# Performance work log

Measured on AMD Instinct MI355X. Metric: run time of the kernel, lower is better.

## Reference

```python
import jax, jax.numpy as jnp
import numpy as np

INPUT_SIZE = 416.0
CONF_THRESH = 0.25
IOU_THRESH = 0.45
N = 8192


def setup_inputs() -> dict:
    key = jax.random.key(0)
    preds = jax.random.normal(key, (1, 5, N), dtype=jnp.float32)
    return {"preds": preds}


def _pairwise_iou(b):
    # b: [N,4] xyxy -> iou: [N,N], matching the torch clamp(min=0) semantics
    xx1 = jnp.maximum(b[:, None, 0], b[None, :, 0])
    yy1 = jnp.maximum(b[:, None, 1], b[None, :, 1])
    xx2 = jnp.minimum(b[:, None, 2], b[None, :, 2])
    yy2 = jnp.minimum(b[:, None, 3], b[None, :, 3])
    inter = jnp.clip(xx2 - xx1, 0.0) * jnp.clip(yy2 - yy1, 0.0)
    area = jnp.clip(b[:, 2] - b[:, 0], 0.0) * jnp.clip(b[:, 3] - b[:, 1], 0.0)  # [N]
    union = area[:, None] + area[None, :] - inter
    return jnp.where(union > 0, inter / union, 0.0)


def reference(preds):
    # decode: preds [1,5,N] rows = (cx, cy, w, h, obj)
    p = preds[0].T  # [N,5]
    cx, cy, pw, ph, obj = p[:, 0], p[:, 1], p[:, 2], p[:, 3], p[:, 4]
    x1 = cx - pw * 0.5
    y1 = cy - ph * 0.5
    x2 = cx + pw * 0.5
    y2 = cy + ph * 0.5
    boxes = jnp.stack([x1, y1, x2, y2], axis=1)  # [N,4]
    scores = obj
    classes = jnp.zeros_like(scores)

    valid = scores > CONF_THRESH  # conf filter (kept as mask; invalid boxes never kept)
    # scale to absolute coords iff all coords are normalized (max <= 1)
    scale = jnp.where(jnp.max(boxes) <= 1.0, INPUT_SIZE, 1.0)
    boxes_abs = boxes * scale

    # greedy NMS over score-descending order
    order = jnp.argsort(-scores)
    b = boxes_abs[order]          # [N,4]
    s = scores[order]             # [N]
    v = valid[order]              # [N]
    c = classes[order]            # [N]

    iou = _pairwise_iou(b)        # [N,N]

    def step(suppressed, xs):
        iou_row, v_i, i = xs
        keep_i = v_i & jnp.logical_not(suppressed[i])
        suppressed = suppressed | (keep_i & (iou_row > IOU_THRESH))
        return suppressed, keep_i

    _, keep = jax.lax.scan(
        step,
        jnp.zeros((N,), dtype=bool),
        (iou, v, jnp.arange(N)),
    )  # keep: [N] bool, in sorted order

    out = jnp.stack(
        [b[:, 0] / INPUT_SIZE, b[:, 1] / INPUT_SIZE,
         b[:, 2] / INPUT_SIZE, b[:, 3] / INPUT_SIZE, s, c],
        axis=1,
    )  # [N,6]
    # fixed-shape jit-compatible output: suppressed/filtered rows are zeroed;
    # kept rows appear in descending-score order (same order torch compacts to)
    return jnp.where(keep[:, None], out, 0.0)
```

## Files before the change

### kernel.cpp

```cpp
#include <hip/hip_runtime.h>
#include <stdint.h>

typedef unsigned long long u64;
typedef unsigned int u32;

#define NBOX 8192
#define ACMAX 1024
#define NCH 16
#define CONF 0.25f
#define IOU_T 0.45f

#define OFF_CX1    256
#define OFF_CY1    (OFF_CX1 + ACMAX * 4)
#define OFF_CX2    (OFF_CX1 + 2 * ACMAX * 4)
#define OFF_CY2    (OFF_CX1 + 3 * ACMAX * 4)
#define OFF_CSC    (OFF_CX1 + 4 * ACMAX * 4)
#define OFF_CAR    (OFF_CX1 + 5 * ACMAX * 4)
#define OFF_ROFC   (OFF_CX1 + 6 * ACMAX * 4)
#define OFF_CMASKT (OFF_CX1 + 7 * ACMAX * 4)

__device__ inline u32 encf(float f) {
    u32 u = __float_as_uint(f);
    return (u & 0x80000000u) ? ~u : (u | 0x80000000u);
}

__global__ void __launch_bounds__(1024) k_sort(
        const float* __restrict__ p,
        float* __restrict__ cx1, float* __restrict__ cy1,
        float* __restrict__ cx2, float* __restrict__ cy2,
        float* __restrict__ csc, float* __restrict__ car,
        int* __restrict__ rofc, float* __restrict__ out) {
    #pragma clang fp contract(off)
    int t = threadIdx.x;
    int b = blockIdx.x;
    __shared__ u64 keys[9216];
    __shared__ u32 accs[128][36];
    __shared__ u32 accs2[8][32];
    __shared__ float redm[16];
    __shared__ float s_gmax;

    int il4 = (t & 7) * 4;
    int js  = t >> 3;
    int ibase = b * 32;

    u64 Ki[4];
    #pragma unroll
    for (int q = 0; q < 4; q++) {
        int i = ibase + il4 + q;
        u32 e = encf(p[4 * NBOX + i]);
        Ki[q] = ((u64)e << 32) | ((u64)(8191 - i) << 19) | 0x1FFFFull;
    }

    float mloc = -3.4e38f;
    #pragma unroll
    for (int w = 0; w < 8; w++) {
        int j = w * 1024 + t;
        float cxj = p[j], cyj = p[NBOX + j];
        float pwj = p[2 * NBOX + j], phj = p[3 * NBOX + j];
        float sj = p[4 * NBOX + j];
        float hx = pwj * 0.5f, hy = phj * 0.5f;
        float x1 = cxj - hx, y1 = cyj - hy, x2 = cxj + hx, y2 = cyj + hy;
        bool act = (sj > CONF) && (x2 > x1) && (y2 > y1);
        mloc = fmaxf(mloc, fmaxf(fmaxf(x1, y1), fmaxf(x2, y2)));
        u32 e = encf(sj);
        u32 mult = act ? 65537u : 1u;
        keys[j + (j >> 3)] =
            ((u64)e << 32) | ((u64)(8191 - j) << 19) | (u64)mult;
    }
    __syncthreads();

    u32 acc[4] = {0u, 0u, 0u, 0u};
    int base = js * 9;
    #pragma unroll
    for (int w = 0; w < 8; w++) {
        #pragma unroll
        for (int m = 0; m < 8; m++) {
            u64 kj = keys[base + w * 1152 + m];
            u32 mm = (u32)kj & 0x1FFFFu;
            acc[0] += (kj > Ki[0]) ? mm : 0u;
            acc[1] += (kj > Ki[1]) ? mm : 0u;
            acc[2] += (kj > Ki[2]) ? mm : 0u;
            acc[3] += (kj > Ki[3]) ? mm : 0u;
        }
    }
    #pragma unroll
    for (int q = 0; q < 4; q++) accs[js][il4 + q] = acc[q];
    #pragma unroll
    for (int o = 32; o > 0; o >>= 1) mloc = fmaxf(mloc, __shfl_xor(mloc, o, 64));
    if ((t & 63) == 0) redm[t >> 6] = mloc;
    __syncthreads();
    if (t < 256) {
        int il = t & 31, part = t >> 5;
        u32 s = 0;
        #pragma unroll
        for (int q = 0; q < 16; q++) s += accs[part * 16 + q][il];
        accs2[part][il] = s;
    }
    if (t == 0) {
        float g = redm[0];
        #pragma unroll
        for (int k = 1; k < 16; k++) g = fmaxf(g, redm[k]);
        s_gmax = g;
    }
    __syncthreads();
    if (t < 32) {
        u32 total = 0;
        #pragma unroll
        for (int part = 0; part < 8; part++) total += accs2[part][t];
        int r = (int)(total & 0xFFFFu);
        int cr = (int)(total >> 16);
        int i = ibase + t;
        float scale = (s_gmax <= 1.0f) ? 416.0f : 1.0f;
        float cx = p[i], cy = p[NBOX + i];
        float pw = p[2 * NBOX + i], ph = p[3 * NBOX + i];
        float s = p[4 * NBOX + i];
        float hx = pw * 0.5f, hy = ph * 0.5f;
        float x1 = cx - hx, y1 = cy - hy, x2 = cx + hx, y2 = cy + hy;
        bool a = (s > CONF) && (x2 > x1) && (y2 > y1);
        float bx1 = x1 * scale, by1 = y1 * scale;
        float bx2 = x2 * scale, by2 = y2 * scale;
        float aw = fmaxf(bx2 - bx1, 0.0f);
        float ah = fmaxf(by2 - by1, 0.0f);
        float area = aw * ah;
        bool ok = a && (cr < ACMAX);
        if (ok) {
            cx1[cr] = bx1; cy1[cr] = by1; cx2[cr] = bx2; cy2[cr] = by2;
            csc[cr] = s; car[cr] = area; rofc[cr] = r;
        } else {
            bool valid = s > CONF;
            float* o = out + (size_t)r * 6;
            o[0] = valid ? bx1 / 416.0f : 0.0f;
            o[1] = valid ? by1 / 416.0f : 0.0f;
            o[2] = valid ? bx2 / 416.0f : 0.0f;
            o[3] = valid ? by2 / 416.0f : 0.0f;
            o[4] = valid ? s : 0.0f;
            o[5] = 0.0f;
        }
    }
}

__global__ void __launch_bounds__(64) k_mask(
        const float* __restrict__ cx1, const float* __restrict__ cy1,
        const float* __restrict__ cx2, const float* __restrict__ cy2,
        const float* __restrict__ car, const float* __restrict__ csc,
        u64* __restrict__ cmaskT) {
    #pragma clang fp contract(off)
    int t = threadIdx.x;
    int i0 = blockIdx.x * 64, j0 = blockIdx.y * 64;
    u64 rv = __ballot(csc[i0 + t] > CONF);
    u64 cv = __ballot(csc[j0 + t] > CONF);
    if (rv == 0ull || cv == 0ull) return;
    __shared__ float sx1[64], sy1[64], sx2[64], sy2[64], sa[64];
    sx1[t] = cx1[i0 + t]; sy1[t] = cy1[i0 + t];
    sx2[t] = cx2[i0 + t]; sy2[t] = cy2[i0 + t];
    sa[t] = car[i0 + t];
    __syncthreads();
    int j = j0 + t;
    float xj1 = cx1[j], yj1 = cy1[j], xj2 = cx2[j], yj2 = cy2[j], aj = car[j];
    u64 w = 0;
    for (int ii = 0; ii < 64; ii++) {
        float xx1 = fmaxf(sx1[ii], xj1);
        float yy1 = fmaxf(sy1[ii], yj1);
        float xx2 = fminf(sx2[ii], xj2);
        float yy2 = fminf(sy2[ii], yj2);
        float iw = fmaxf(xx2 - xx1, 0.0f);
        float ih = fmaxf(yy2 - yy1, 0.0f);
        float inter = iw * ih;
        float uni = sa[ii] + aj - inter;
        bool sup = (uni > 0.0f) && (inter / uni > IOU_T);
        w |= ((u64)(sup ? 1u : 0u)) << ii;
    }
    cmaskT[(size_t)blockIdx.x * ACMAX + j] = w;
}

__global__ void __launch_bounds__(1024) k_final(
        const float* __restrict__ csc, const u64* __restrict__ cmaskT,
        const float* __restrict__ cx1, const float* __restrict__ cy1,
        const float* __restrict__ cx2, const float* __restrict__ cy2,
        const int* __restrict__ rofc, float* __restrict__ out) {
    int t = threadIdx.x;
    __shared__ u64 keptArr[NCH];
    int wv = t >> 6;
    int j = t & 63;
    float s = csc[t];
    bool valid = s > CONF;
    u64 col[NCH];
    #pragma unroll
    for (int w = 0; w < NCH; w++) col[w] = cmaskT[(size_t)w * ACMAX + t];
    u64 validm = __ballot(valid);
    if (j == 0) keptArr[wv] = validm;
    __syncthreads();
    u64 below = (j == 0) ? 0ull : (~0ull >> (64 - j));
    for (int iter = 0; iter < 1024; ++iter) {
        bool sup = false;
        for (int w = 0; w < wv; ++w)
            sup |= (col[w] & keptArr[w]) != 0ull;
        sup |= (col[wv] & keptArr[wv] & below) != 0ull;
        u64 nk = validm & ~__ballot(sup);
        int ch = (nk != keptArr[wv]) ? 1 : 0;
        __syncthreads();
        if (j == 0) keptArr[wv] = nk;
        if (!__syncthreads_or(ch)) break;
    }
    if (valid) {
        bool kb = (keptArr[wv] >> j) & 1ull;
        int r = rofc[t];
        float* o = out + (size_t)r * 6;
        o[0] = kb ? cx1[t] / 416.0f : 0.0f;
        o[1] = kb ? cy1[t] / 416.0f : 0.0f;
        o[2] = kb ? cx2[t] / 416.0f : 0.0f;
        o[3] = kb ? cy2[t] / 416.0f : 0.0f;
        o[4] = kb ? s : 0.0f;
        o[5] = 0.0f;
    }
}

extern "C" void kernel_launch(void* const* d_in, const int* in_sizes, int n_in,
                              void* d_out, int out_size, void* d_ws, size_t ws_size,
                              hipStream_t stream) {
    const float* preds = (const float*)d_in[0];
    float* out = (float*)d_out;
    char* ws = (char*)d_ws;
    float* cx1 = (float*)(ws + OFF_CX1);
    float* cy1 = (float*)(ws + OFF_CY1);
    float* cx2 = (float*)(ws + OFF_CX2);
    float* cy2 = (float*)(ws + OFF_CY2);
    float* csc = (float*)(ws + OFF_CSC);
    float* car = (float*)(ws + OFF_CAR);
    int* rofc  = (int*)(ws + OFF_ROFC);
    u64* cmaskT = (u64*)(ws + OFF_CMASKT);

    hipLaunchKernelGGL(k_sort, dim3(256), dim3(1024), 0, stream,
                       preds, cx1, cy1, cx2, cy2, csc, car, rofc, out);
    hipLaunchKernelGGL(k_mask, dim3(NCH, NCH), dim3(64), 0, stream,
                       cx1, cy1, cx2, cy2, car, csc, cmaskT);
    hipLaunchKernelGGL(k_final, dim3(1), dim3(1024), 0, stream,
                       csc, cmaskT, cx1, cy1, cx2, cy2, rofc, out);
}
```

Baseline: 93.04 us.

## Fuse mask and final NMS kernels with last-block-done atomic ticket

Merges the IoU mask kernel and the single-block greedy suppression kernel into one launch of 16 blocks of 1024 threads. Each block computes one row chunk of the mask, and the last block to finish, found through an atomic counter, runs the suppression loop. This removes one kernel launch and its inter-kernel gap. In exchange the mask work now runs on fewer, larger blocks and adds a fence, an atomic and a counter reset in k_sort.

```diff
diff --git a/kernel.cpp b/kernel.cpp
--- a/kernel.cpp
+++ b/kernel.cpp
@@ -10,6 +10,7 @@
 #define CONF 0.25f
 #define IOU_T 0.45f
 
+#define OFF_DONE   0
 #define OFF_CX1    256
 #define OFF_CY1    (OFF_CX1 + ACMAX * 4)
 #define OFF_CX2    (OFF_CX1 + 2 * ACMAX * 4)
@@ -29,10 +30,12 @@
         float* __restrict__ cx1, float* __restrict__ cy1,
         float* __restrict__ cx2, float* __restrict__ cy2,
         float* __restrict__ csc, float* __restrict__ car,
-        int* __restrict__ rofc, float* __restrict__ out) {
+        int* __restrict__ rofc, float* __restrict__ out,
+        u32* __restrict__ doneCnt) {
     #pragma clang fp contract(off)
     int t = threadIdx.x;
     int b = blockIdx.x;
+    if (b == 0 && t == 0) *doneCnt = 0u;
     __shared__ u64 keys[9216];
     __shared__ u32 accs[128][36];
     __shared__ u32 accs2[8][32];
@@ -139,58 +142,67 @@
     }
 }
 
-__global__ void __launch_bounds__(64) k_mask(
+__global__ void __launch_bounds__(1024) k_maskfinal(
         const float* __restrict__ cx1, const float* __restrict__ cy1,
         const float* __restrict__ cx2, const float* __restrict__ cy2,
         const float* __restrict__ car, const float* __restrict__ csc,
-        u64* __restrict__ cmaskT) {
+        const int* __restrict__ rofc, u64* __restrict__ cmaskT,
+        u32* __restrict__ doneCnt, float* __restrict__ out) {
     #pragma clang fp contract(off)
     int t = threadIdx.x;
-    int i0 = blockIdx.x * 64, j0 = blockIdx.y * 64;
-    u64 rv = __ballot(csc[i0 + t] > CONF);
-    u64 cv = __ballot(csc[j0 + t] > CONF);
-    if (rv == 0ull || cv == 0ull) return;
+    int b = blockIdx.x;
     __shared__ float sx1[64], sy1[64], sx2[64], sy2[64], sa[64];
-    sx1[t] = cx1[i0 + t]; sy1[t] = cy1[i0 + t];
-    sx2[t] = cx2[i0 + t]; sy2[t] = cy2[i0 + t];
-    sa[t] = car[i0 + t];
-    __syncthreads();
-    int j = j0 + t;
-    float xj1 = cx1[j], yj1 = cy1[j], xj2 = cx2[j], yj2 = cy2[j], aj = car[j];
-    u64 w = 0;
-    for (int ii = 0; ii < 64; ii++) {
-        float xx1 = fmaxf(sx1[ii], xj1);
-        float yy1 = fmaxf(sy1[ii], yj1);
-        float xx2 = fminf(sx2[ii], xj2);
-        float yy2 = fminf(sy2[ii], yj2);
-        float iw = fmaxf(xx2 - xx1, 0.0f);
-        float ih = fmaxf(yy2 - yy1, 0.0f);
-        float inter = iw * ih;
-        float uni = sa[ii] + aj - inter;
-        bool sup = (uni > 0.0f) && (inter / uni > IOU_T);
-        w |= ((u64)(sup ? 1u : 0u)) << ii;
-    }
-    cmaskT[(size_t)blockIdx.x * ACMAX + j] = w;
-}
-
-__global__ void __launch_bounds__(1024) k_final(
-        const float* __restrict__ csc, const u64* __restrict__ cmaskT,
-        const float* __restrict__ cx1, const float* __restrict__ cy1,
-        const float* __restrict__ cx2, const float* __restrict__ cy2,
-        const int* __restrict__ rofc, float* __restrict__ out) {
-    int t = threadIdx.x;
+    __shared__ u32 s_ticket;
     __shared__ u64 keptArr[NCH];
+
+    if (t < 64) {
+        sx1[t] = cx1[b * 64 + t]; sy1[t] = cy1[b * 64 + t];
+        sx2[t] = cx2[b * 64 + t]; sy2[t] = cy2[b * 64 + t];
+        sa[t]  = car[b * 64 + t];
+    }
+    __syncthreads();
+    int lane = t & 63;
+    int j = t;
+    u64 rv = __ballot(csc[b * 64 + lane] > CONF);
+    u64 cv = __ballot(csc[j] > CONF);
+    if (rv != 0ull && cv != 0ull) {
+        float xj1 = cx1[j], yj1 = cy1[j];
+        float xj2 = cx2[j], yj2 = cy2[j], aj = car[j];
+        u64 w = 0;
+        for (int ii = 0; ii < 64; ii++) {
+            float xx1 = fmaxf(sx1[ii], xj1);
+            float yy1 = fmaxf(sy1[ii], yj1);
+            float xx2 = fminf(sx2[ii], xj2);
+            float yy2 = fminf(sy2[ii], yj2);
+            float iw = fmaxf(xx2 - xx1, 0.0f);
+            float ih = fmaxf(yy2 - yy1, 0.0f);
+            float inter = iw * ih;
+            float uni = sa[ii] + aj - inter;
+            bool sup = (uni > 0.0f) && (inter / uni > IOU_T);
+            w |= ((u64)(sup ? 1u : 0u)) << ii;
+        }
+        cmaskT[(size_t)b * ACMAX + j] = w;
+    }
+    __syncthreads();
+    __threadfence();
+    if (t == 0) {
+        s_ticket = __hip_atomic_fetch_add(doneCnt, 1u, __ATOMIC_ACQ_REL,
+                                          __HIP_MEMORY_SCOPE_AGENT);
+    }
+    __syncthreads();
+    if (s_ticket != 15u) return;
+
     int wv = t >> 6;
-    int j = t & 63;
     float s = csc[t];
     bool valid = s > CONF;
     u64 col[NCH];
     #pragma unroll
     for (int w = 0; w < NCH; w++) col[w] = cmaskT[(size_t)w * ACMAX + t];
     u64 validm = __ballot(valid);
-    if (j == 0) keptArr[wv] = validm;
-    __syncthreads();
-    u64 below = (j == 0) ? 0ull : (~0ull >> (64 - j));
+    if ((t & 63) == 0) keptArr[wv] = validm;
+    __syncthreads();
+    int jj = t & 63;
+    u64 below = (jj == 0) ? 0ull : (~0ull >> (64 - jj));
     for (int iter = 0; iter < 1024; ++iter) {
         bool sup = false;
         for (int w = 0; w < wv; ++w)
@@ -199,11 +211,11 @@
         u64 nk = validm & ~__ballot(sup);
         int ch = (nk != keptArr[wv]) ? 1 : 0;
         __syncthreads();
-        if (j == 0) keptArr[wv] = nk;
+        if (jj == 0) keptArr[wv] = nk;
         if (!__syncthreads_or(ch)) break;
     }
     if (valid) {
-        bool kb = (keptArr[wv] >> j) & 1ull;
+        bool kb = (keptArr[wv] >> jj) & 1ull;
         int r = rofc[t];
         float* o = out + (size_t)r * 6;
         o[0] = kb ? cx1[t] / 416.0f : 0.0f;
@@ -221,6 +233,7 @@
     const float* preds = (const float*)d_in[0];
     float* out = (float*)d_out;
     char* ws = (char*)d_ws;
+    u32* doneCnt = (u32*)(ws + OFF_DONE);
     float* cx1 = (float*)(ws + OFF_CX1);
     float* cy1 = (float*)(ws + OFF_CY1);
     float* cx2 = (float*)(ws + OFF_CX2);
@@ -231,9 +244,7 @@
     u64* cmaskT = (u64*)(ws + OFF_CMASKT);
 
     hipLaunchKernelGGL(k_sort, dim3(256), dim3(1024), 0, stream,
-                       preds, cx1, cy1, cx2, cy2, csc, car, rofc, out);
-    hipLaunchKernelGGL(k_mask, dim3(NCH, NCH), dim3(64), 0, stream,
-                       cx1, cy1, cx2, cy2, car, csc, cmaskT);
-    hipLaunchKernelGGL(k_final, dim3(1), dim3(1024), 0, stream,
-                       csc, cmaskT, cx1, cy1, cx2, cy2, rofc, out);
-}
+                       preds, cx1, cy1, cx2, cy2, csc, car, rofc, out, doneCnt);
+    hipLaunchKernelGGL(k_maskfinal, dim3(16), dim3(1024), 0, stream,
+                       cx1, cy1, cx2, cy2, car, csc, rofc, cmaskT, doneCnt, out);
+}
```

Result: slower. 102.1 us (+9.8%).
